# Kernel optimization log

Measured on AMD Instinct MI355X. Metric: run time of the kernel, lower is better.

The kernel has to match this reference:

```python
import jax, jax.numpy as jnp
import numpy as np

# Hyperparams matching init_kwargs
KH = KW = KL = 3
SH = SW = SL = 1
PH = PW = PL = 1
DH = DW = DL = 1
DG = 1  # deformable_groups


def _out_dim(s, pad, dil, k, stride):
    return (s + 2 * pad - (dil * (k - 1) + 1)) // stride + 1


def _deform_conv3d(x, offset, mask, weight):
    # x: [N, C, H, W, L]; weight: [Cout, C//groups, KH, KW, KL] (groups=1)
    N, C, H, W, L = x.shape
    Cout = weight.shape[0]
    kprod = KH * KW * KL
    Ho = _out_dim(H, PH, DH, KH, SH)
    Wo = _out_dim(W, PW, DW, KW, SW)
    Lo = _out_dim(L, PL, DL, KL, SL)

    # offset layout: [N, DG, kprod, 3(h,w,l), Ho, Wo, Lo]; mask: [N, DG, kprod, Ho, Wo, Lo]
    off = offset.reshape(N, DG, kprod, 3, Ho, Wo, Lo)
    m = mask.reshape(N, DG, kprod, Ho, Wo, Lo)

    # kernel tap positions (kidx = i*KW*KL + j*KL + k), scaled by dilation
    ki, kj, kk = jnp.meshgrid(jnp.arange(KH), jnp.arange(KW), jnp.arange(KL), indexing='ij')
    kh = (ki.reshape(-1) * DH).astype(jnp.float32)  # [kprod]
    kw = (kj.reshape(-1) * DW).astype(jnp.float32)
    kl = (kk.reshape(-1) * DL).astype(jnp.float32)

    hb = (jnp.arange(Ho) * SH - PH).astype(jnp.float32)
    wb = (jnp.arange(Wo) * SW - PW).astype(jnp.float32)
    lb = (jnp.arange(Lo) * SL - PL).astype(jnp.float32)

    # sampling coordinates: [N, DG, kprod, Ho, Wo, Lo]
    ch = off[:, :, :, 0] + hb[None, None, None, :, None, None] + kh[None, None, :, None, None, None]
    cw = off[:, :, :, 1] + wb[None, None, None, None, :, None] + kw[None, None, :, None, None, None]
    cl = off[:, :, :, 2] + lb[None, None, None, None, None, :] + kl[None, None, :, None, None, None]

    Cpg = C // DG
    xf = x.reshape(N, DG, Cpg, H * W * L)
    P = kprod * Ho * Wo * Lo

    h0 = jnp.floor(ch); w0 = jnp.floor(cw); l0 = jnp.floor(cl)
    fh = ch - h0; fw = cw - w0; fl = cl - l0
    h0i = h0.astype(jnp.int32); w0i = w0.astype(jnp.int32); l0i = l0.astype(jnp.int32)

    # trilinear interpolation: accumulate over 8 corners (zero outside volume)
    val = jnp.zeros((N, DG, Cpg, P), x.dtype)
    for dh in (0, 1):
        for dw in (0, 1):
            for dl in (0, 1):
                ih = h0i + dh; iw = w0i + dw; il = l0i + dl
                wgt = (fh if dh else 1.0 - fh) * (fw if dw else 1.0 - fw) * (fl if dl else 1.0 - fl)
                valid = (ih >= 0) & (ih < H) & (iw >= 0) & (iw < W) & (il >= 0) & (il < L)
                lin = ((jnp.clip(ih, 0, H - 1) * W + jnp.clip(iw, 0, W - 1)) * L
                       + jnp.clip(il, 0, L - 1)).reshape(N, DG, 1, P)
                g = jnp.take_along_axis(xf, jnp.broadcast_to(lin, (N, DG, Cpg, P)), axis=3)
                val = val + g * (wgt * valid).reshape(N, DG, 1, P)

    # modulate by mask, then contract columns with weight (groups=1)
    val = val.reshape(N, DG, Cpg, kprod, Ho, Wo, Lo) * m[:, :, None]
    cols = val.reshape(N, C, kprod, Ho * Wo * Lo)
    out = jnp.einsum('nckp,ock->nop', cols, weight.reshape(Cout, C, kprod))
    return out.reshape(N, Cout, Ho, Wo, Lo)


def setup_inputs() -> dict:
    key = jax.random.key(0)
    k1, k2, k3, k4 = jax.random.split(key, 4)
    N, C, H, W, L = 1, 64, 32, 32, 32
    Cout = 64
    kprod = KH * KW * KL
    Ho = _out_dim(H, PH, DH, KH, SH)
    Wo = _out_dim(W, PW, DW, KW, SW)
    Lo = _out_dim(L, PL, DL, KL, SL)
    x = jax.random.normal(k1, (N, C, H, W, L), jnp.float32)
    offset = jax.random.normal(k2, (N, DG * 3 * kprod, Ho, Wo, Lo), jnp.float32)
    mask = jax.random.uniform(k3, (N, DG * kprod, Ho, Wo, Lo), jnp.float32)
    stdv = 1.0 / np.sqrt(C * kprod)
    weight = jax.random.uniform(k4, (Cout, C, KH, KW, KL), jnp.float32, -stdv, stdv)
    return {"x": x, "offset": offset, "mask": mask, "weight": weight}


def reference(x, offset, mask, weight):
    return _deform_conv3d(x, offset, mask, weight)
```

## Files before the change

### kernel.cpp

```cpp
#include <hip/hip_runtime.h>
#include <hip/hip_bf16.h>

typedef short short8 __attribute__((ext_vector_type(8)));
typedef unsigned int u32x4 __attribute__((ext_vector_type(4)));
typedef float f32x4 __attribute__((ext_vector_type(4)));
typedef float f32x2 __attribute__((ext_vector_type(2)));

#define SPAT  32768
#define KPROD 27

__device__ __constant__ float4 KTAB[KPROD] = {
    {0,0,0,0},{0,0,1,0},{0,0,2,0},{0,1,0,0},{0,1,1,0},{0,1,2,0},{0,2,0,0},{0,2,1,0},{0,2,2,0},
    {1,0,0,0},{1,0,1,0},{1,0,2,0},{1,1,0,0},{1,1,1,0},{1,1,2,0},{1,2,0,0},{1,2,1,0},{1,2,2,0},
    {2,0,0,0},{2,0,1,0},{2,0,2,0},{2,1,0,0},{2,1,1,0},{2,1,2,0},{2,2,0,0},{2,2,1,0},{2,2,2,0}
};

static __device__ __forceinline__ short f2bf(float f) {
    return (short)__bfloat16_as_ushort(__float2bfloat16(f));
}

template<int S>
static __device__ __forceinline__ int qbcast_i(int x) {
    return __builtin_amdgcn_mov_dpp(x, S * 0x55, 0xF, 0xF, true);
}
template<int S>
static __device__ __forceinline__ float qbcast_f(float x) {
    return __int_as_float(qbcast_i<S>(__float_as_int(x)));
}

__global__ void transpose_x_bf16(const float* __restrict__ x, unsigned short* __restrict__ xt) {
    __shared__ float tile[64][65];
    const int t = threadIdx.x;
    const int s0 = blockIdx.x * 64;
    const int lane = t & 63, grp = t >> 6;
#pragma unroll
    for (int r = 0; r < 16; ++r) {
        int c = grp * 16 + r;
        tile[c][lane] = x[c * SPAT + s0 + lane];
    }
    __syncthreads();
#pragma unroll
    for (int r = 0; r < 16; ++r) {
        int srow = grp * 16 + r;
        xt[(s0 + srow) * 64 + lane] = __bfloat16_as_ushort(__float2bfloat16(tile[lane][srow]));
    }
}

__global__ void prep_w_frag(const float* __restrict__ w, unsigned short* __restrict__ wt) {
    int idx = blockIdx.x * 256 + threadIdx.x;
    if (idx >= KPROD * 4096) return;
    int k = idx >> 12;
    int fid = idx & 4095;
    int i = fid >> 9;
    int lane = (fid >> 3) & 63;
    int e = fid & 7;
    int ot = i >> 1, kb = i & 1;
    int o = ot * 16 + (lane & 15);
    int c = kb * 32 + (lane >> 4) * 8 + e;
    wt[idx] = __bfloat16_as_ushort(__float2bfloat16(w[(o * 64 + c) * KPROD + k]));
}

__global__ __launch_bounds__(128)
void dconv3d_ktab(const unsigned short* __restrict__ xt, const unsigned short* __restrict__ wf,
                  const float* __restrict__ offset, const float* __restrict__ mask,
                  float* __restrict__ out) {
    __shared__ float red[16][65];

    const int t    = threadIdx.x;
    const int wid  = t >> 6;
    const int l    = t & 63;
    const int pl   = l & 15;
    const int g    = l >> 4;
    const int gp   = l >> 2;
    const int gg   = l & 3;
    const int dhq  = gg >> 1, dwq = gg & 1;
    const int goff = wid * 64 + gg * 16;
    const int bpidx = (pl * 4 + g) * 4;

    const int nwg = (int)gridDim.x;
    const int cpx = nwg >> 3;
    const int bid = (int)blockIdx.x;
    const int bsw = (bid & 7) * cpx + (bid >> 3);

    const int p_base = bsw * 16;
    const int pos_g = p_base + gp;
    const int hog = pos_g >> 10, wog = (pos_g >> 5) & 31, log = pos_g & 31;
    const float fho = (float)(hog - 1), fwo = (float)(wog - 1), flo = (float)(log - 1);
    const char* xbase = (const char*)xt;

    f32x4 acc[4] = {};

    auto load_off = [&](int k) -> f32x4 {
        f32x4 r;
        r.x = offset[(3 * k + 0) * SPAT + pos_g];
        r.y = offset[(3 * k + 1) * SPAT + pos_g];
        r.z = offset[(3 * k + 2) * SPAT + pos_g];
        r.w = mask[k * SPAT + pos_g];
        return r;
    };

    auto compute_meta = [&](int k, f32x4 om, float w01[2], int o01[2]) {
        float4 kt = KTAB[k];
        float chh = om.x + (fho + kt.x);
        float cww = om.y + (fwo + kt.y);
        float cll = om.z + (flo + kt.z);
        float h0f = floorf(chh), w0f = floorf(cww), l0f = floorf(cll);
        float fh = chh - h0f, fw = cww - w0f, fl = cll - l0f;
        int h0 = (int)h0f, w0 = (int)w0f, l0i = (int)l0f;
        int ih = h0 + dhq, iw = w0 + dwq;
        float wh = dhq ? fh : 1.f - fh;
        float ww = dwq ? fw : 1.f - fw;
        float whwm = wh * ww * om.w;
        float w1v = whwm * fl;
        float w0v = whwm - w1v;
        bool vhw = ((unsigned)ih < 32u) && ((unsigned)iw < 32u);
        bool v0 = vhw && ((unsigned)l0i < 32u);
        bool v1 = vhw && ((unsigned)(l0i + 1) < 32u);
        w01[0] = v0 ? w0v : 0.f;
        w01[1] = v1 ? w1v : 0.f;
        int ihc = min(max(ih, 0), 31), iwc = min(max(iw, 0), 31);
        int l0c = min(max(l0i, 0), 31);
        int l1c = min(max(l0i + 1, 0), 31);
        int base2 = (ihc * 32 + iwc) * 32;
        o01[0] = (((base2 + l0c) << 7) + goff);
        o01[1] = (((base2 + l1c) << 7) + goff);
    };

    auto exchange = [&](const float w01[2], const int o01[2], float mwO[8], int moO[8]) {
        mwO[0] = qbcast_f<0>(w01[0]); mwO[1] = qbcast_f<0>(w01[1]);
        mwO[2] = qbcast_f<1>(w01[0]); mwO[3] = qbcast_f<1>(w01[1]);
        mwO[4] = qbcast_f<2>(w01[0]); mwO[5] = qbcast_f<2>(w01[1]);
        mwO[6] = qbcast_f<3>(w01[0]); mwO[7] = qbcast_f<3>(w01[1]);
        moO[0] = qbcast_i<0>(o01[0]); moO[1] = qbcast_i<0>(o01[1]);
        moO[2] = qbcast_i<1>(o01[0]); moO[3] = qbcast_i<1>(o01[1]);
        moO[4] = qbcast_i<2>(o01[0]); moO[5] = qbcast_i<2>(o01[1]);
        moO[6] = qbcast_i<3>(o01[0]); moO[7] = qbcast_i<3>(o01[1]);
    };


    const char* xgg = xbase + goff;

    float mw[8];
    u32x4 q[8];
    {
        f32x4 om0 = load_off(0);
        float w01[2]; int o01[2], mo0[8];
        compute_meta(0, om0, w01, o01);
        o01[0] -= goff; o01[1] -= goff;
        exchange(w01, o01, mw, mo0);
#pragma unroll
        for (int j = 0; j < 8; ++j)
            q[j] = *(const u32x4*)(xgg + mo0[j]);
    }
    f32x4 offA = load_off(1);

#pragma unroll 1
    for (int k = 0; k < KPROD; ++k) {
        short8 wfr[4];
#pragma unroll
        for (int ot = 0; ot < 4; ++ot)
            wfr[ot] = *(const short8*)&wf[((size_t)k * 8 + ot * 2 + wid) * 512 + l * 8];

        f32x4 offB;
        if (k + 2 < KPROD) offB = load_off(k + 2);

        float mwN[8]; int moN[8];
        if (k + 1 < KPROD) {
            float w01[2]; int o01[2];
            compute_meta(k + 1, offA, w01, o01);
            o01[0] -= goff; o01[1] -= goff;
            exchange(w01, o01, mwN, moN);
        }

        f32x2 v[4] = {};
#pragma unroll
        for (int j = 0; j < 8; ++j) {
            f32x2 w2 = {mw[j], mw[j]};
#pragma unroll
            for (int qd = 0; qd < 4; ++qd) {
                unsigned int a = q[j][qd];
                f32x2 xa = {__uint_as_float(a << 16), __uint_as_float(a & 0xffff0000u)};
                v[qd] = __builtin_elementwise_fma(w2, xa, v[qd]);
            }
        }
        union { short8 s; u32x4 u; } bg;
#pragma unroll
        for (int qd = 0; qd < 4; ++qd) {
            bg.s[2 * qd]     = f2bf(v[qd].x);
            bg.s[2 * qd + 1] = f2bf(v[qd].y);
        }

        if (k + 1 < KPROD) {
#pragma unroll
            for (int j = 0; j < 8; ++j)
                q[j] = *(const u32x4*)(xgg + moN[j]);
        }

        union { u32x4 u; short8 s; } bm;
#pragma unroll
        for (int d = 0; d < 4; ++d)
            bm.u[d] = (unsigned)__builtin_amdgcn_ds_bpermute(bpidx, (int)bg.u[d]);

#pragma unroll
        for (int ot = 0; ot < 4; ++ot)
            acc[ot] = __builtin_amdgcn_mfma_f32_16x16x32_bf16(wfr[ot], bm.s, acc[ot], 0, 0, 0);

        if (k + 1 < KPROD) {
#pragma unroll
            for (int j = 0; j < 8; ++j) mw[j] = mwN[j];
        }
        offA = offB;
    }

    __syncthreads();
    if (wid == 0) {
#pragma unroll
        for (int ot = 0; ot < 4; ++ot)
#pragma unroll
            for (int r = 0; r < 4; ++r)
                red[pl][ot * 16 + g * 4 + r] = acc[ot][r];
    }
    __syncthreads();
    if (wid == 1) {
#pragma unroll
        for (int ot = 0; ot < 4; ++ot)
#pragma unroll
            for (int r = 0; r < 4; ++r)
                red[pl][ot * 16 + g * 4 + r] += acc[ot][r];
    }
    __syncthreads();

#pragma unroll
    for (int it = 0; it < 8; ++it) {
        int idx = it * 128 + t;
        int p = idx & 15, o = idx >> 4;
        out[(size_t)o * SPAT + p_base + p] = red[p][o];
    }
}

extern "C" void kernel_launch(void* const* d_in, const int* in_sizes, int n_in,
                              void* d_out, int out_size, void* d_ws, size_t ws_size,
                              hipStream_t stream) {
    const float* x      = (const float*)d_in[0];
    const float* offset = (const float*)d_in[1];
    const float* mask   = (const float*)d_in[2];
    const float* weight = (const float*)d_in[3];
    float* out = (float*)d_out;

    unsigned short* xt  = (unsigned short*)d_ws;
    unsigned short* wtb = (unsigned short*)((char*)d_ws + (size_t)SPAT * 64 * 2);

    hipLaunchKernelGGL(transpose_x_bf16, dim3(SPAT / 64), dim3(256), 0, stream, x, xt);
    hipLaunchKernelGGL(prep_w_frag, dim3((KPROD * 4096 + 255) / 256), dim3(256), 0, stream,
                       weight, wtb);
    hipLaunchKernelGGL(dconv3d_ktab, dim3(SPAT / 16), dim3(128), 0, stream,
                       xt, wtb, offset, mask, out);
}
```

Baseline: 86.46 us.

## Split kernel taps across two block groups with partial output reduction

Divides the 27 kernel taps into two groups (14 and 13) along a second grid dimension, so twice as many workgroups each run a shorter tap loop. The second group writes to a workspace partial buffer, which a new reduce_add kernel then adds into the output. This is meant to raise parallelism and occupancy, or shorten the per-block serial chain. In exchange it adds an extra launch and an 8 MB read-modify-write pass, and it only takes effect when the workspace is large enough.

```diff
diff --git a/kernel.cpp b/kernel.cpp
--- a/kernel.cpp
+++ b/kernel.cpp
@@ -61,9 +61,9 @@
 }
 
 __global__ __launch_bounds__(128)
-void dconv3d_ktab(const unsigned short* __restrict__ xt, const unsigned short* __restrict__ wf,
-                  const float* __restrict__ offset, const float* __restrict__ mask,
-                  float* __restrict__ out) {
+void dconv3d_ks(const unsigned short* __restrict__ xt, const unsigned short* __restrict__ wf,
+                const float* __restrict__ offset, const float* __restrict__ mask,
+                float* __restrict__ out0, float* __restrict__ out1, int ngroups) {
     __shared__ float red[16][65];
 
     const int t    = threadIdx.x;
@@ -77,6 +77,11 @@
     const int goff = wid * 64 + gg * 16;
     const int bpidx = (pl * 4 + g) * 4;
 
+    const int grpid = (ngroups == 2) ? (int)blockIdx.y : 0;
+    const int k0 = (ngroups == 2) ? grpid * 14 : 0;
+    const int nt = (ngroups == 2) ? (14 - grpid) : KPROD;
+    float* outp = (grpid == 0) ? out0 : out1;
+
     const int nwg = (int)gridDim.x;
     const int cpx = nwg >> 3;
     const int bid = (int)blockIdx.x;
@@ -87,6 +92,7 @@
     const int hog = pos_g >> 10, wog = (pos_g >> 5) & 31, log = pos_g & 31;
     const float fho = (float)(hog - 1), fwo = (float)(wog - 1), flo = (float)(log - 1);
     const char* xbase = (const char*)xt;
+    const char* xgg = xbase + goff;
 
     f32x4 acc[4] = {};
 
@@ -122,8 +128,8 @@
         int l0c = min(max(l0i, 0), 31);
         int l1c = min(max(l0i + 1, 0), 31);
         int base2 = (ihc * 32 + iwc) * 32;
-        o01[0] = (((base2 + l0c) << 7) + goff);
-        o01[1] = (((base2 + l1c) << 7) + goff);
+        o01[0] = (base2 + l0c) << 7;
+        o01[1] = (base2 + l1c) << 7;
     };
 
     auto exchange = [&](const float w01[2], const int o01[2], float mwO[8], int moO[8]) {
@@ -137,38 +143,35 @@
         moO[6] = qbcast_i<3>(o01[0]); moO[7] = qbcast_i<3>(o01[1]);
     };
 
-
-    const char* xgg = xbase + goff;
-
     float mw[8];
     u32x4 q[8];
     {
-        f32x4 om0 = load_off(0);
+        f32x4 om0 = load_off(k0);
         float w01[2]; int o01[2], mo0[8];
-        compute_meta(0, om0, w01, o01);
-        o01[0] -= goff; o01[1] -= goff;
+        compute_meta(k0, om0, w01, o01);
         exchange(w01, o01, mw, mo0);
 #pragma unroll
         for (int j = 0; j < 8; ++j)
             q[j] = *(const u32x4*)(xgg + mo0[j]);
     }
-    f32x4 offA = load_off(1);
+    f32x4 offA = load_off(k0 + 1);
 
 #pragma unroll 1
-    for (int k = 0; k < KPROD; ++k) {
+    for (int kk = 0; kk < nt; ++kk) {
+        const int k = k0 + kk;
+
         short8 wfr[4];
 #pragma unroll
         for (int ot = 0; ot < 4; ++ot)
             wfr[ot] = *(const short8*)&wf[((size_t)k * 8 + ot * 2 + wid) * 512 + l * 8];
 
         f32x4 offB;
-        if (k + 2 < KPROD) offB = load_off(k + 2);
+        if (kk + 2 < nt) offB = load_off(k + 2);
 
         float mwN[8]; int moN[8];
-        if (k + 1 < KPROD) {
+        if (kk + 1 < nt) {
             float w01[2]; int o01[2];
             compute_meta(k + 1, offA, w01, o01);
-            o01[0] -= goff; o01[1] -= goff;
             exchange(w01, o01, mwN, moN);
         }
 
@@ -190,7 +193,7 @@
             bg.s[2 * qd + 1] = f2bf(v[qd].y);
         }
 
-        if (k + 1 < KPROD) {
+        if (kk + 1 < nt) {
 #pragma unroll
             for (int j = 0; j < 8; ++j)
                 q[j] = *(const u32x4*)(xgg + moN[j]);
@@ -205,7 +208,7 @@
         for (int ot = 0; ot < 4; ++ot)
             acc[ot] = __builtin_amdgcn_mfma_f32_16x16x32_bf16(wfr[ot], bm.s, acc[ot], 0, 0, 0);
 
-        if (k + 1 < KPROD) {
+        if (kk + 1 < nt) {
 #pragma unroll
             for (int j = 0; j < 8; ++j) mw[j] = mwN[j];
         }
@@ -234,8 +237,16 @@
     for (int it = 0; it < 8; ++it) {
         int idx = it * 128 + t;
         int p = idx & 15, o = idx >> 4;
-        out[(size_t)o * SPAT + p_base + p] = red[p][o];
-    }
+        outp[(size_t)o * SPAT + p_base + p] = red[p][o];
+    }
+}
+
+__global__ void reduce_add(float* __restrict__ out, const float* __restrict__ part) {
+    int i = blockIdx.x * 256 + threadIdx.x;
+    f32x4 a = ((const f32x4*)out)[i];
+    f32x4 b = ((const f32x4*)part)[i];
+    a.x += b.x; a.y += b.y; a.z += b.z; a.w += b.w;
+    ((f32x4*)out)[i] = a;
 }
 
 extern "C" void kernel_launch(void* const* d_in, const int* in_sizes, int n_in,
@@ -247,12 +258,23 @@
     const float* weight = (const float*)d_in[3];
     float* out = (float*)d_out;
 
+    const size_t xt_bytes  = (size_t)SPAT * 64 * 2;
+    const size_t wt_bytes  = (size_t)KPROD * 4096 * 2;
+    const size_t prt_bytes = (size_t)64 * SPAT * 4;
+
     unsigned short* xt  = (unsigned short*)d_ws;
-    unsigned short* wtb = (unsigned short*)((char*)d_ws + (size_t)SPAT * 64 * 2);
+    unsigned short* wtb = (unsigned short*)((char*)d_ws + xt_bytes);
+    float*          prt = (float*)((char*)d_ws + xt_bytes + wt_bytes);
+
+    const bool split = (ws_size >= xt_bytes + wt_bytes + prt_bytes);
+    const int ngroups = split ? 2 : 1;
 
     hipLaunchKernelGGL(transpose_x_bf16, dim3(SPAT / 64), dim3(256), 0, stream, x, xt);
     hipLaunchKernelGGL(prep_w_frag, dim3((KPROD * 4096 + 255) / 256), dim3(256), 0, stream,
                        weight, wtb);
-    hipLaunchKernelGGL(dconv3d_ktab, dim3(SPAT / 16), dim3(128), 0, stream,
-                       xt, wtb, offset, mask, out);
-}
+    hipLaunchKernelGGL(dconv3d_ks, dim3(SPAT / 16, ngroups), dim3(128), 0, stream,
+                       xt, wtb, offset, mask, out, prt, ngroups);
+    if (split)
+        hipLaunchKernelGGL(reduce_add, dim3(64 * SPAT / 4 / 256), dim3(256), 0, stream,
+                           out, prt);
+}
```

After: 82.95 us, median of 2. -4.1%, faster.
